# Optimization experiments

Hardware: AMD Instinct MI355X
Metric: run time of the kernel (lower is better)

## Reference

```python
import jax, jax.numpy as jnp
import numpy as np

B, S, D, H = 4, 1024, 1024, 16
HD = D // H


def setup_inputs() -> dict:
    key = jax.random.key(0)
    ks = jax.random.split(key, 12)
    s = 1.0 / np.sqrt(D)
    inp = {
        'q': jax.random.normal(ks[0], (B, S, D), jnp.float32),
        'k': jax.random.normal(ks[1], (B, S, D), jnp.float32),
        'v': jax.random.normal(ks[2], (B, S, D), jnp.float32),
        'mask': jnp.broadcast_to(jnp.tril(jnp.ones((S, S), jnp.int32)), (B, S, S)),
        'Wq': jax.random.uniform(ks[3], (D, D), jnp.float32, -s, s),
        'bq': jax.random.uniform(ks[4], (D,), jnp.float32, -s, s),
        'Wk': jax.random.uniform(ks[5], (D, D), jnp.float32, -s, s),
        'bk': jax.random.uniform(ks[6], (D,), jnp.float32, -s, s),
        'Wv': jax.random.uniform(ks[7], (D, D), jnp.float32, -s, s),
        'bv': jax.random.uniform(ks[8], (D,), jnp.float32, -s, s),
        'Wo': jax.random.uniform(ks[9], (D, D), jnp.float32, -s, s),
        'bo': jax.random.uniform(ks[10], (D,), jnp.float32, -s, s),
    }
    return inp


def _split_heads(x):
    # [B,S,D] -> [B,H,S,HD]
    b, s, d = x.shape
    return x.reshape(b, s, H, HD).transpose(0, 2, 1, 3)


def reference(q, k, v, mask, Wq, bq, Wk, bk, Wv, bv, Wo, bo):
    # Linear projections (torch Linear: x @ W.T + b) followed by relu
    qh = jax.nn.relu(q @ Wq.T + bq)
    kh = jax.nn.relu(k @ Wk.T + bk)
    vh = jax.nn.relu(v @ Wv.T + bv)
    qh, kh, vh = _split_heads(qh), _split_heads(kh), _split_heads(vh)
    scores = jnp.einsum('bhqd,bhkd->bhqk', qh, kh) / jnp.sqrt(jnp.float32(HD))
    scores = jnp.where(mask[:, None, :, :] == 0, jnp.float32(-1e9), scores)
    attn = jax.nn.softmax(scores, axis=-1)
    y = jnp.einsum('bhqk,bhkd->bhqd', attn, vh)
    y = y.transpose(0, 2, 1, 3).reshape(B, S, D)  # merge heads
    return jax.nn.relu(y @ Wo.T + bo)
```

## Files before the change

kernel.cpp:

```cpp
#include <hip/hip_runtime.h>


using f16    = _Float16;
using f16x4  = __attribute__((ext_vector_type(4))) _Float16;
using f16x8  = __attribute__((ext_vector_type(8))) _Float16;
using f32x4  = __attribute__((ext_vector_type(4))) float;
using f32x16 = __attribute__((ext_vector_type(16))) float;

static constexpr int S = 1024, Dm = 1024, NH = 16, HD = 64;

#if __has_builtin(__builtin_amdgcn_mfma_f32_32x32x16_f16)
#define USE_G32 1
#define MFMA32(ACC, A_, B_) \
    (ACC) = __builtin_amdgcn_mfma_f32_32x32x16_f16((A_), (B_), (ACC), 0, 0, 0)
#else
#define USE_G32 0
#endif

#if __has_builtin(__builtin_amdgcn_mfma_f32_16x16x32_f16) && \
    __has_builtin(__builtin_amdgcn_mfma_f32_16x16x16f16)
#define USE_A16 1
#define MFMA16K32(ACC, A_, B_) \
    (ACC) = __builtin_amdgcn_mfma_f32_16x16x32_f16((A_), (B_), (ACC), 0, 0, 0)
#define MFMA16(ACC, A_, B_) \
    (ACC) = __builtin_amdgcn_mfma_f32_16x16x16f16((A_), (B_), (ACC), 0, 0, 0)
#else
#define USE_A16 0
#endif

#define LO4(v) __builtin_shufflevector((v), (v), 0, 1, 2, 3)
#define HI4(v) __builtin_shufflevector((v), (v), 4, 5, 6, 7)

__device__ __forceinline__ f16x4 cvt4(float4 a) {
    f16x4 r; r[0] = (f16)a.x; r[1] = (f16)a.y; r[2] = (f16)a.z; r[3] = (f16)a.w;
    return r;
}

__device__ __forceinline__ int pcol64(int k) {
#if USE_A16
    return ((k >> 3) & 3) * 16 + ((k >> 5) << 3) + (k & 7);
#else
    return ((k >> 2) & 3) * 16 + ((k >> 4) << 2) + (k & 3);
#endif
}

__device__ __forceinline__ int swz(int row, int col) {
    return (col & ~31) | ((((col >> 3) ^ (row >> 1)) & 3) << 3) | (col & 7);
}

__device__ __forceinline__ void store_out(void* out, int mode, int m, int n, float v) {
    const int b_ = m >> 10, s_ = m & 1023, h_ = n >> 6, hd_ = n & 63;
    const size_t idx = (mode == 0)
        ? (((size_t)(b_ * NH + h_) * S + s_) * HD + pcol64(hd_))
        : (((size_t)(b_ * NH + h_) * HD + hd_) * S + s_);
    ((f16*)out)[idx] = (f16)v;
}

#if __has_builtin(__builtin_amdgcn_global_load_lds)
#define HAS_GLL 1
#else
#define HAS_GLL 0
#endif

__device__ __forceinline__ void gll16(const void* g, void* l) {
#if HAS_GLL
    __builtin_amdgcn_global_load_lds(
        (const __attribute__((address_space(1))) void*)g,
        (__attribute__((address_space(3))) void*)l, 16, 0, 0);
#else
    *(uint4*)l = *(const uint4*)g;
#endif
}

__global__ __launch_bounds__(256)
void cvt_w(const float* __restrict__ s0, const float* __restrict__ s1,
           const float* __restrict__ s2, f16* __restrict__ dst)
{
    const int z = blockIdx.y;
    const float* src = (z == 0) ? s0 : (z == 1) ? s1 : s2;
    const int e = blockIdx.x * 256 + threadIdx.x;
    const int n = e >> 8;
    const int k = (e & 255) * 4;
    const float4 v = *(const float4*)(src + (size_t)n * Dm + k);
    *(f16x4*)(dst + (size_t)z * Dm * Dm + (size_t)n * Dm + swz(n, k)) = cvt4(v);
}

__global__ __launch_bounds__(256, 3)
void gemm_qkv(const float* __restrict__ q, const float* __restrict__ k,
              const float* __restrict__ v, const f16* __restrict__ wqkv,
              const float* __restrict__ bq, const float* __restrict__ bk,
              const float* __restrict__ bv,
              f16* __restrict__ qh, f16* __restrict__ kh, f16* __restrict__ vt)
{
    const int z = blockIdx.z;
    const float* A = (z == 0) ? q : (z == 1) ? k : v;
    const float* bias = (z == 0) ? bq : (z == 1) ? bk : bv;
    f16* out = (z == 0) ? qh : (z == 1) ? kh : vt;
    const int mode = (z == 2) ? 1 : 0;
    const f16* Wf = wqkv + (size_t)z * Dm * Dm;

    const int tid = threadIdx.x;
    const int bm = blockIdx.x, bn = blockIdx.y;
#if USE_G32
    __shared__ alignas(16) float As[2][128][32];
    __shared__ alignas(16) f16   Ws[2][128][32];

    const int lane = tid & 63, wave = tid >> 6;
    const int l31 = lane & 31, kh2 = lane >> 5;
    const int wm = wave & 1, wn = wave >> 1;

    const int arow = tid >> 3;
    const int aslotD = tid & 7;
    const int aslotS = aslotD ^ (arow & 7);
    const float* Asrc0 = A + (size_t)(bm * 128 + arow) * Dm + aslotS * 4;
    const int wrow = tid >> 2, wcol = (tid & 3) * 8;
    const f16* Wsrc0 = Wf + (size_t)(bn * 128 + wrow) * Dm + wcol;

    auto dma = [&](int k0, int buf) {
#pragma unroll
        for (int ch = 0; ch < 4; ++ch)
            gll16(Asrc0 + (size_t)ch * 32 * Dm + k0,
                  &As[buf][ch * 32 + arow][aslotD * 4]);
        gll16(Wsrc0 + k0,                    &Ws[buf][wrow][wcol]);
        gll16(Wsrc0 + (size_t)64 * Dm + k0,  &Ws[buf][64 + wrow][wcol]);
    };

    auto afrag = [&](int buf, int r, int s) -> f16x8 {
        const int p = s * 4 + kh2 * 2, r7 = r & 7;
        const f32x4 lo = *(const f32x4*)&As[buf][r][(p ^ r7) * 4];
        const f32x4 hi = *(const f32x4*)&As[buf][r][((p + 1) ^ r7) * 4];
        f16x8 f;
        f[0] = (f16)lo[0]; f[1] = (f16)lo[1]; f[2] = (f16)lo[2]; f[3] = (f16)lo[3];
        f[4] = (f16)hi[0]; f[5] = (f16)hi[1]; f[6] = (f16)hi[2]; f[7] = (f16)hi[3];
        return f;
    };
    auto wfrag = [&](int buf, int r, int s) -> f16x8 {
        const int sl = s * 2 + kh2;
        return *(const f16x8*)&Ws[buf][r][((sl ^ (r >> 1)) & 3) * 8];
    };

    f32x16 acc[2][2] = {};
    auto kslice = [&](int buf, int s) {
        const f16x8 af0 = afrag(buf, wm * 64 + l31, s);
        const f16x8 af1 = afrag(buf, wm * 64 + 32 + l31, s);
        const f16x8 bf0 = wfrag(buf, wn * 64 + l31, s);
        const f16x8 bf1 = wfrag(buf, wn * 64 + 32 + l31, s);
        MFMA32(acc[0][0], af0, bf0);
        MFMA32(acc[0][1], af0, bf1);
        MFMA32(acc[1][0], af1, bf0);
        MFMA32(acc[1][1], af1, bf1);
    };

    constexpr int NIT = Dm / 32;
    dma(0, 0);
    for (int t = 0; t < NIT; ++t) {
        const int cur = t & 1;
        __syncthreads();
        if (t + 1 < NIT) dma((t + 1) * 32, cur ^ 1);
        kslice(cur, 0);
        kslice(cur, 1);
    }

#pragma unroll
    for (int g2 = 0; g2 < 2; ++g2) {
        const int col = bn * 128 + wn * 64 + g2 * 32 + l31;
        const float bb = bias[col];
#pragma unroll
        for (int g = 0; g < 2; ++g)
#pragma unroll
            for (int blk = 0; blk < 4; ++blk) {
                const int row0 = bm * 128 + wm * 64 + g * 32 + 8 * blk + 4 * kh2;
                if (mode == 1) {
                    const int b_ = row0 >> 10, s_ = row0 & 1023;
                    const int h_ = col >> 6, hd_ = col & 63;
                    f16x4 vv;
#pragma unroll
                    for (int r = 0; r < 4; ++r)
                        vv[r] = (f16)fmaxf(acc[g][g2][blk * 4 + r] + bb, 0.0f);
                    *(f16x4*)&out[((size_t)(b_ * NH + h_) * HD + hd_) * S + s_] = vv;
                } else {
#pragma unroll
                    for (int r = 0; r < 4; ++r)
                        store_out(out, mode, row0 + r, col,
                                  fmaxf(acc[g][g2][blk * 4 + r] + bb, 0.0f));
                }
            }
    }
#else
    for (int i = tid; i < 128 * 128; i += 256) {
        const int m = bm * 128 + (i >> 7);
        const int n = bn * 128 + (i & 127);
        float acc = 0.0f;
        for (int k2 = 0; k2 < Dm; ++k2)
            acc = fmaf(A[(size_t)m * Dm + k2], (float)Wf[(size_t)n * Dm + swz(n, k2)], acc);
        store_out(out, mode, m, n, fmaxf(acc + bias[n], 0.0f));
    }
#endif
}

__global__ __launch_bounds__(256, 4)
void gemm_out(const f16* __restrict__ y, const f16* __restrict__ wo,
              const float* __restrict__ bo, float* __restrict__ out)
{
    const int tid = threadIdx.x;
    const int bm = blockIdx.x, bn = blockIdx.y;
#if USE_G32
    __shared__ alignas(16) f16 As[2][64][32];
    __shared__ alignas(16) f16 Ws[2][64][32];

    const int lane = tid & 63, wave = tid >> 6;
    const int l31 = lane & 31, kh2 = lane >> 5;
    const int wm = wave & 1, wn = wave >> 1;

    const int drow = tid >> 2, dcol = (tid & 3) * 8;
    const f16* Asrc = y  + (size_t)(bm * 64 + drow) * Dm + dcol;
    const f16* Wsrc = wo + (size_t)(bn * 64 + drow) * Dm + dcol;

    auto dma = [&](int k0, int buf) {
        gll16(Asrc + k0, &As[buf][drow][dcol]);
        gll16(Wsrc + k0, &Ws[buf][drow][dcol]);
    };
    auto frag = [&](const f16 (&L)[64][32], int r, int s) -> f16x8 {
        const int sl = s * 2 + kh2;
        return *(const f16x8*)&L[r][((sl ^ (r >> 1)) & 3) * 8];
    };

    f32x16 acc = {};
    constexpr int NIT = Dm / 32;
    dma(0, 0);
    for (int t = 0; t < NIT; ++t) {
        const int cur = t & 1;
        __syncthreads();
        if (t + 1 < NIT) dma((t + 1) * 32, cur ^ 1);
#pragma unroll
        for (int s = 0; s < 2; ++s) {
            const f16x8 af = frag(As[cur], wm * 32 + l31, s);
            const f16x8 bf = frag(Ws[cur], wn * 32 + l31, s);
            MFMA32(acc, af, bf);
        }
    }

    const int col = bn * 64 + wn * 32 + l31;
    const float bb = bo[col];
#pragma unroll
    for (int blk = 0; blk < 4; ++blk) {
        const int row0 = bm * 64 + wm * 32 + 8 * blk + 4 * kh2;
#pragma unroll
        for (int r = 0; r < 4; ++r)
            out[(size_t)(row0 + r) * Dm + col] = fmaxf(acc[blk * 4 + r] + bb, 0.0f);
    }
#else
    for (int i = tid; i < 64 * 64; i += 256) {
        const int m = bm * 64 + (i >> 6);
        const int n = bn * 64 + (i & 63);
        float acc = 0.0f;
        for (int k2 = 0; k2 < Dm; ++k2)
            acc = fmaf((float)y[(size_t)m * Dm + swz(m, k2)],
                       (float)wo[(size_t)n * Dm + swz(n, k2)], acc);
        out[(size_t)m * Dm + n] = fmaxf(acc + bo[n], 0.0f);
    }
#endif
}

__global__ __launch_bounds__(256)
void attn_fwd(const f16* __restrict__ qh, const f16* __restrict__ kh,
              const f16* __restrict__ vt, f16* __restrict__ y)
{
    const int bz = blockIdx.x;
    const int qt = bz & 15;
    const int h  = (bz >> 4) & 15;
    const int b  = bz >> 8;
    const size_t head = (size_t)(b * NH + h) * S * HD;

#if USE_A16
    __shared__ alignas(16) f16 Ks[2][64][72];
    __shared__ alignas(16) f16 Vs[2][64][72];

    const int tid  = threadIdx.x;
    const int wave = tid >> 6;
    const int lane = tid & 63;
    const int l15  = lane & 15;
    const int quad = lane >> 4;
    const int sr   = tid >> 2;
    const int sc   = (tid & 3) * 16;

    const f16* Qrow = qh + head + (size_t)(qt * 64 + wave * 16 + l15) * HD;
    const f16* Kp   = kh + head;
    const f16* Vp   = vt + head;

    f16x8 aq[2];
    {
        const uint4 q0 = *(const uint4*)(Qrow + quad * 16);
        const uint4 q1 = *(const uint4*)(Qrow + quad * 16 + 8);
        aq[0] = *(f16x8*)&q0;
        aq[1] = *(f16x8*)&q1;
    }

    const int qg = qt * 64 + wave * 16 + l15;
    float m_i = -1e30f, l_i = 0.0f;
    f32x4 acc_o[4] = {};

    uint4 pk[2], pv[2];
    auto pref = [&](int kt) {
        const f16* Kr = Kp + (size_t)(kt * 64 + sr) * HD + sc;
        pk[0] = *(const uint4*)Kr;
        pk[1] = *(const uint4*)(Kr + 8);
        const f16* Vr = Vp + (size_t)sr * S + kt * 64 + sc;
        pv[0] = *(const uint4*)Vr;
        pv[1] = *(const uint4*)(Vr + 8);
    };

    pref(0);
    for (int kt = 0; kt <= qt; ++kt) {
        const int cur = kt & 1;
        *(uint4*)&Ks[cur][sr][sc]     = pk[0];
        *(uint4*)&Ks[cur][sr][sc + 8] = pk[1];
        {
            const int sb = (sc >> 4) * 4;
            *(f16x4*)&Vs[cur][sr][0 * 16 + sb] = *(f16x4*)((f16*)&pv[0]);
            *(f16x4*)&Vs[cur][sr][1 * 16 + sb] = *(f16x4*)((f16*)&pv[0] + 4);
            *(f16x4*)&Vs[cur][sr][2 * 16 + sb] = *(f16x4*)((f16*)&pv[1]);
            *(f16x4*)&Vs[cur][sr][3 * 16 + sb] = *(f16x4*)((f16*)&pv[1] + 4);
        }
        __syncthreads();
        if (kt < qt) pref(kt + 1);

        f32x4 accs[4] = {};
#pragma unroll
        for (int t = 0; t < 4; ++t) {
            const f16x8 k8a = *(const f16x8*)&Ks[cur][t * 16 + l15][quad * 16];
            const f16x8 k8b = *(const f16x8*)&Ks[cur][t * 16 + l15][quad * 16 + 8];
            MFMA16K32(accs[t], k8a, aq[0]);
            MFMA16K32(accs[t], k8b, aq[1]);
        }

        const int key0 = kt * 64 + quad * 4;
#pragma unroll
        for (int t = 0; t < 4; ++t)
#pragma unroll
            for (int r = 0; r < 4; ++r) {
                float sv = accs[t][r] * 0.125f;
                if (key0 + t * 16 + r > qg) sv = -1e9f;
                accs[t][r] = sv;
            }

        float mx = accs[0][0];
#pragma unroll
        for (int t = 0; t < 4; ++t)
#pragma unroll
            for (int r = 0; r < 4; ++r) mx = fmaxf(mx, accs[t][r]);
        mx = fmaxf(mx, __shfl_xor(mx, 16, 64));
        mx = fmaxf(mx, __shfl_xor(mx, 32, 64));
        const float mnew = fmaxf(m_i, mx);
        float sm = 0.0f;
#pragma unroll
        for (int t = 0; t < 4; ++t)
#pragma unroll
            for (int r = 0; r < 4; ++r) {
                const float e = __expf(accs[t][r] - mnew);
                accs[t][r] = e;
                sm += e;
            }
        sm += __shfl_xor(sm, 16, 64);
        sm += __shfl_xor(sm, 32, 64);
        const float alpha = __expf(m_i - mnew);
        l_i = l_i * alpha + sm;
        m_i = mnew;

        f16x4 ap[4];
#pragma unroll
        for (int c = 0; c < 4; ++c) {
            f16x4 v;
#pragma unroll
            for (int j = 0; j < 4; ++j) v[j] = (f16)accs[c][j];
            ap[c] = v;
        }

        float ar[4];
#pragma unroll
        for (int r = 0; r < 4; ++r) ar[r] = __shfl(alpha, quad * 4 + r, 64);
#pragma unroll
        for (int t2 = 0; t2 < 4; ++t2)
#pragma unroll
            for (int r = 0; r < 4; ++r) acc_o[t2][r] *= ar[r];
#pragma unroll
        for (int t2 = 0; t2 < 4; ++t2) {
            const f16x8 v8a = *(const f16x8*)&Vs[cur][t2 * 16 + l15][quad * 16];
            const f16x8 v8b = *(const f16x8*)&Vs[cur][t2 * 16 + l15][quad * 16 + 8];
            MFMA16(acc_o[t2], ap[0], LO4(v8a));
            MFMA16(acc_o[t2], ap[1], HI4(v8a));
            MFMA16(acc_o[t2], ap[2], LO4(v8b));
            MFMA16(acc_o[t2], ap[3], HI4(v8b));
        }
    }

    float lr[4];
#pragma unroll
    for (int r = 0; r < 4; ++r) lr[r] = __shfl(l_i, quad * 4 + r, 64);
#pragma unroll
    for (int t2 = 0; t2 < 4; ++t2)
#pragma unroll
        for (int r = 0; r < 4; ++r) {
            const int srow = qt * 64 + wave * 16 + quad * 4 + r;
            const int dcol = h * 64 + t2 * 16 + l15;
            y[((size_t)b * S + srow) * Dm + swz(srow, dcol)] =
                (f16)(acc_o[t2][r] / lr[r]);
        }
#else
    const int tid = threadIdx.x;
    if (tid < 64) {
        const int q = qt * 64 + tid;
        const f16* Qr = qh + head + (size_t)q * HD;
        float qv[64];
        for (int d = 0; d < 64; ++d) qv[d] = (float)Qr[pcol64(d)];
        float mx = -1e30f;
        for (int key = 0; key <= q; ++key) {
            const f16* Kr = kh + head + (size_t)key * HD;
            float s = 0.0f;
            for (int d = 0; d < 64; ++d) s = fmaf(qv[d], (float)Kr[pcol64(d)], s);
            mx = fmaxf(mx, s * 0.125f);
        }
        float o[64];
        for (int d = 0; d < 64; ++d) o[d] = 0.0f;
        float l = 0.0f;
        for (int key = 0; key <= q; ++key) {
            const f16* Kr = kh + head + (size_t)key * HD;
            float s = 0.0f;
            for (int d = 0; d < 64; ++d) s = fmaf(qv[d], (float)Kr[pcol64(d)], s);
            const float p = __expf(s * 0.125f - mx);
            l += p;
            for (int d = 0; d < 64; ++d)
                o[d] = fmaf(p, (float)vt[head + (size_t)d * S + key], o[d]);
        }
        for (int d = 0; d < 64; ++d)
            y[((size_t)b * S + q) * Dm + swz(q, h * 64 + d)] = (f16)(o[d] / l);
    }
#endif
}

extern "C" void kernel_launch(void* const* d_in, const int* in_sizes, int n_in,
                              void* d_out, int out_size, void* d_ws, size_t ws_size,
                              hipStream_t stream)
{
    f16* ws = (f16*)d_ws;
    const size_t SEG = (size_t)4 * 1024 * 1024;
    f16* qh   = ws;
    f16* kh   = ws + SEG;
    f16* vt   = ws + 2 * SEG;
    f16* wqkv = ws + 3 * SEG;
    f16* y    = ws + 3 * SEG;
    f16* wo   = ws;

    cvt_w<<<dim3(1024, 3), 256, 0, stream>>>(
        (const float*)d_in[4], (const float*)d_in[6], (const float*)d_in[8], wqkv);
    gemm_qkv<<<dim3(32, 8, 3), 256, 0, stream>>>(
        (const float*)d_in[0], (const float*)d_in[1], (const float*)d_in[2],
        wqkv,
        (const float*)d_in[5], (const float*)d_in[7], (const float*)d_in[9],
        qh, kh, vt);
    attn_fwd<<<dim3(4 * NH * (S / 64)), 256, 0, stream>>>(qh, kh, vt, y);
    cvt_w<<<dim3(1024, 1), 256, 0, stream>>>(
        (const float*)d_in[10], nullptr, nullptr, wo);
    gemm_out<<<dim3(64, 16), 256, 0, stream>>>(
        y, wo, (const float*)d_in[11], (float*)d_out);
}
```

Before: 253.5 us.

## Widen QKV GEMM to 512 threads and fuse Wo fp16 conversion into output GEMM

The QKV projection GEMM now runs 8 waves per 128x128 tile, each wave owning a 32x64 sub-tile with two accumulators instead of four. The aim is more latency hiding and lower register pressure per wave. The output projection GEMM now loads the fp32 Wo directly into shared memory through a swizzled layout and converts it to fp16 while building fragments. This removes the separate cvt_w launch and the workspace round trip for Wo, at the cost of double the LDS traffic for W and per-k conversion work in every block.

New measurement: 251.2 us. About the same (-0.9%).

```diff
diff --git a/kernel.cpp b/kernel.cpp
--- a/kernel.cpp
+++ b/kernel.cpp
@@ -85,7 +85,7 @@
     *(f16x4*)(dst + (size_t)z * Dm * Dm + (size_t)n * Dm + swz(n, k)) = cvt4(v);
 }
 
-__global__ __launch_bounds__(256, 3)
+__global__ __launch_bounds__(512, 6)
 void gemm_qkv(const float* __restrict__ q, const float* __restrict__ k,
               const float* __restrict__ v, const f16* __restrict__ wqkv,
               const float* __restrict__ bq, const float* __restrict__ bk,
@@ -107,7 +107,7 @@
 
     const int lane = tid & 63, wave = tid >> 6;
     const int l31 = lane & 31, kh2 = lane >> 5;
-    const int wm = wave & 1, wn = wave >> 1;
+    const int wm = wave & 3, wn = wave >> 2;
 
     const int arow = tid >> 3;
     const int aslotD = tid & 7;
@@ -117,12 +117,9 @@
     const f16* Wsrc0 = Wf + (size_t)(bn * 128 + wrow) * Dm + wcol;
 
     auto dma = [&](int k0, int buf) {
-#pragma unroll
-        for (int ch = 0; ch < 4; ++ch)
-            gll16(Asrc0 + (size_t)ch * 32 * Dm + k0,
-                  &As[buf][ch * 32 + arow][aslotD * 4]);
-        gll16(Wsrc0 + k0,                    &Ws[buf][wrow][wcol]);
-        gll16(Wsrc0 + (size_t)64 * Dm + k0,  &Ws[buf][64 + wrow][wcol]);
+        gll16(Asrc0 + k0,                      &As[buf][arow][aslotD * 4]);
+        gll16(Asrc0 + (size_t)64 * Dm + k0,    &As[buf][64 + arow][aslotD * 4]);
+        gll16(Wsrc0 + k0,                      &Ws[buf][wrow][wcol]);
     };
 
     auto afrag = [&](int buf, int r, int s) -> f16x8 {
@@ -139,16 +136,13 @@
         return *(const f16x8*)&Ws[buf][r][((sl ^ (r >> 1)) & 3) * 8];
     };
 
-    f32x16 acc[2][2] = {};
+    f32x16 acc[2] = {};
     auto kslice = [&](int buf, int s) {
-        const f16x8 af0 = afrag(buf, wm * 64 + l31, s);
-        const f16x8 af1 = afrag(buf, wm * 64 + 32 + l31, s);
+        const f16x8 af  = afrag(buf, wm * 32 + l31, s);
         const f16x8 bf0 = wfrag(buf, wn * 64 + l31, s);
         const f16x8 bf1 = wfrag(buf, wn * 64 + 32 + l31, s);
-        MFMA32(acc[0][0], af0, bf0);
-        MFMA32(acc[0][1], af0, bf1);
-        MFMA32(acc[1][0], af1, bf0);
-        MFMA32(acc[1][1], af1, bf1);
+        MFMA32(acc[0], af, bf0);
+        MFMA32(acc[1], af, bf1);
     };
 
     constexpr int NIT = Dm / 32;
@@ -162,32 +156,30 @@
     }
 
 #pragma unroll
-    for (int g2 = 0; g2 < 2; ++g2) {
-        const int col = bn * 128 + wn * 64 + g2 * 32 + l31;
+    for (int j = 0; j < 2; ++j) {
+        const int col = bn * 128 + wn * 64 + j * 32 + l31;
         const float bb = bias[col];
 #pragma unroll
-        for (int g = 0; g < 2; ++g)
-#pragma unroll
-            for (int blk = 0; blk < 4; ++blk) {
-                const int row0 = bm * 128 + wm * 64 + g * 32 + 8 * blk + 4 * kh2;
-                if (mode == 1) {
-                    const int b_ = row0 >> 10, s_ = row0 & 1023;
-                    const int h_ = col >> 6, hd_ = col & 63;
-                    f16x4 vv;
-#pragma unroll
-                    for (int r = 0; r < 4; ++r)
-                        vv[r] = (f16)fmaxf(acc[g][g2][blk * 4 + r] + bb, 0.0f);
-                    *(f16x4*)&out[((size_t)(b_ * NH + h_) * HD + hd_) * S + s_] = vv;
-                } else {
-#pragma unroll
-                    for (int r = 0; r < 4; ++r)
-                        store_out(out, mode, row0 + r, col,
-                                  fmaxf(acc[g][g2][blk * 4 + r] + bb, 0.0f));
-                }
+        for (int blk = 0; blk < 4; ++blk) {
+            const int row0 = bm * 128 + wm * 32 + 8 * blk + 4 * kh2;
+            if (mode == 1) {
+                const int b_ = row0 >> 10, s_ = row0 & 1023;
+                const int h_ = col >> 6, hd_ = col & 63;
+                f16x4 vv;
+#pragma unroll
+                for (int r = 0; r < 4; ++r)
+                    vv[r] = (f16)fmaxf(acc[j][blk * 4 + r] + bb, 0.0f);
+                *(f16x4*)&out[((size_t)(b_ * NH + h_) * HD + hd_) * S + s_] = vv;
+            } else {
+#pragma unroll
+                for (int r = 0; r < 4; ++r)
+                    store_out(out, mode, row0 + r, col,
+                              fmaxf(acc[j][blk * 4 + r] + bb, 0.0f));
             }
-    }
-#else
-    for (int i = tid; i < 128 * 128; i += 256) {
+        }
+    }
+#else
+    for (int i = tid; i < 128 * 128; i += 512) {
         const int m = bm * 128 + (i >> 7);
         const int n = bn * 128 + (i & 127);
         float acc = 0.0f;
@@ -198,31 +190,44 @@
 #endif
 }
 
-__global__ __launch_bounds__(256, 4)
-void gemm_out(const f16* __restrict__ y, const f16* __restrict__ wo,
+__global__ __launch_bounds__(256, 6)
+void gemm_out(const f16* __restrict__ y, const float* __restrict__ wo,
               const float* __restrict__ bo, float* __restrict__ out)
 {
     const int tid = threadIdx.x;
     const int bm = blockIdx.x, bn = blockIdx.y;
 #if USE_G32
-    __shared__ alignas(16) f16 As[2][64][32];
-    __shared__ alignas(16) f16 Ws[2][64][32];
+    __shared__ alignas(16) f16   As[2][64][32];
+    __shared__ alignas(16) float Wsf[2][64][32];
 
     const int lane = tid & 63, wave = tid >> 6;
     const int l31 = lane & 31, kh2 = lane >> 5;
     const int wm = wave & 1, wn = wave >> 1;
 
     const int drow = tid >> 2, dcol = (tid & 3) * 8;
-    const f16* Asrc = y  + (size_t)(bm * 64 + drow) * Dm + dcol;
-    const f16* Wsrc = wo + (size_t)(bn * 64 + drow) * Dm + dcol;
+    const f16* Asrc = y + (size_t)(bm * 64 + drow) * Dm + dcol;
+    const int wrow = tid >> 3;
+    const int wslotD = tid & 7;
+    const int wslotS = wslotD ^ (wrow & 7);
+    const float* Wsrc0 = wo + (size_t)(bn * 64 + wrow) * Dm + wslotS * 4;
 
     auto dma = [&](int k0, int buf) {
         gll16(Asrc + k0, &As[buf][drow][dcol]);
-        gll16(Wsrc + k0, &Ws[buf][drow][dcol]);
-    };
-    auto frag = [&](const f16 (&L)[64][32], int r, int s) -> f16x8 {
+        gll16(Wsrc0 + k0,                   &Wsf[buf][wrow][wslotD * 4]);
+        gll16(Wsrc0 + (size_t)32 * Dm + k0, &Wsf[buf][32 + wrow][wslotD * 4]);
+    };
+    auto yfrag = [&](int buf, int r, int s) -> f16x8 {
         const int sl = s * 2 + kh2;
-        return *(const f16x8*)&L[r][((sl ^ (r >> 1)) & 3) * 8];
+        return *(const f16x8*)&As[buf][r][((sl ^ (r >> 1)) & 3) * 8];
+    };
+    auto wfrag32 = [&](int buf, int r, int s) -> f16x8 {
+        const int p = s * 4 + kh2 * 2, r7 = r & 7;
+        const f32x4 lo = *(const f32x4*)&Wsf[buf][r][(p ^ r7) * 4];
+        const f32x4 hi = *(const f32x4*)&Wsf[buf][r][((p + 1) ^ r7) * 4];
+        f16x8 f;
+        f[0] = (f16)lo[0]; f[1] = (f16)lo[1]; f[2] = (f16)lo[2]; f[3] = (f16)lo[3];
+        f[4] = (f16)hi[0]; f[5] = (f16)hi[1]; f[6] = (f16)hi[2]; f[7] = (f16)hi[3];
+        return f;
     };
 
     f32x16 acc = {};
@@ -234,8 +239,8 @@
         if (t + 1 < NIT) dma((t + 1) * 32, cur ^ 1);
 #pragma unroll
         for (int s = 0; s < 2; ++s) {
-            const f16x8 af = frag(As[cur], wm * 32 + l31, s);
-            const f16x8 bf = frag(Ws[cur], wn * 32 + l31, s);
+            const f16x8 af = yfrag(cur, wm * 32 + l31, s);
+            const f16x8 bf = wfrag32(cur, wn * 32 + l31, s);
             MFMA32(acc, af, bf);
         }
     }
@@ -256,7 +261,7 @@
         float acc = 0.0f;
         for (int k2 = 0; k2 < Dm; ++k2)
             acc = fmaf((float)y[(size_t)m * Dm + swz(m, k2)],
-                       (float)wo[(size_t)n * Dm + swz(n, k2)], acc);
+                       wo[(size_t)n * Dm + k2], acc);
         out[(size_t)m * Dm + n] = fmaxf(acc + bo[n], 0.0f);
     }
 #endif
@@ -449,18 +454,15 @@
     f16* vt   = ws + 2 * SEG;
     f16* wqkv = ws + 3 * SEG;
     f16* y    = ws + 3 * SEG;
-    f16* wo   = ws;
 
     cvt_w<<<dim3(1024, 3), 256, 0, stream>>>(
         (const float*)d_in[4], (const float*)d_in[6], (const float*)d_in[8], wqkv);
-    gemm_qkv<<<dim3(32, 8, 3), 256, 0, stream>>>(
+    gemm_qkv<<<dim3(32, 8, 3), 512, 0, stream>>>(
         (const float*)d_in[0], (const float*)d_in[1], (const float*)d_in[2],
         wqkv,
         (const float*)d_in[5], (const float*)d_in[7], (const float*)d_in[9],
         qh, kh, vt);
     attn_fwd<<<dim3(4 * NH * (S / 64)), 256, 0, stream>>>(qh, kh, vt, y);
-    cvt_w<<<dim3(1024, 1), 256, 0, stream>>>(
-        (const float*)d_in[10], nullptr, nullptr, wo);
     gemm_out<<<dim3(64, 16), 256, 0, stream>>>(
-        y, wo, (const float*)d_in[11], (float*)d_out);
-}
+        y, (const float*)d_in[10], (const float*)d_in[11], (float*)d_out);
+}
```
